# Performance work log

Hardware: AMD Instinct MI355X
Metric: run time of the kernel (lower is better)

The kernel has to match this reference:

```python
import jax, jax.numpy as jnp
import numpy as np

N_NODES = 50000
N_EDGES = 400000
D = 512
LN_EPS = 1e-5


def setup_inputs() -> dict:
    key = jax.random.key(0)
    k0, k1, k2, k3 = jax.random.split(key, 4)
    x = jax.random.normal(k0, (N_NODES, D), dtype=jnp.float32)
    src = jax.random.randint(k1, (N_EDGES,), 0, N_NODES, dtype=jnp.int64)
    dst = jax.random.randint(k2, (N_EDGES,), 0, N_NODES, dtype=jnp.int64)
    W = jax.random.normal(k3, (D, D), dtype=jnp.float32) * 0.05
    b = jnp.zeros((D,), dtype=jnp.float32)
    gamma = jnp.ones((D,), dtype=jnp.float32)
    beta = jnp.zeros((D,), dtype=jnp.float32)
    return {"x": x, "W": W, "b": b, "gamma": gamma, "beta": beta, "src": src, "dst": dst}


def reference(x, W, b, gamma, beta, src, dst):
    n = x.shape[0]
    ones = jnp.ones(src.shape, dtype=x.dtype)
    # DGL GraphConv norm='both': clamp degrees to >= 1
    deg_out = jnp.clip(jax.ops.segment_sum(ones, src, num_segments=n), 1.0)  # [N]
    deg_in = jnp.clip(jax.ops.segment_sum(ones, dst, num_segments=n), 1.0)   # [N]
    h = x * jax.lax.rsqrt(deg_out)[:, None]                 # [N, D] src normalization
    agg = jax.ops.segment_sum(h[src], dst, num_segments=n)  # gather->scatter-add SpMM
    h = agg * jax.lax.rsqrt(deg_in)[:, None]                # dst normalization
    h = h @ W + b                                           # dense linear
    # LayerNorm over last dim
    mu = jnp.mean(h, axis=-1, keepdims=True)
    var = jnp.mean(jnp.square(h - mu), axis=-1, keepdims=True)
    h = (h - mu) * jax.lax.rsqrt(var + LN_EPS) * gamma + beta
    # torch nn.GELU default = exact erf GELU
    return jax.nn.gelu(h, approximate=False)
```

## Files before the change

kernel.cpp:

```cpp
#include <hip/hip_runtime.h>
#include <hip/hip_bf16.h>

#define D 512

typedef __attribute__((ext_vector_type(8))) short bf16x8;
typedef __attribute__((ext_vector_type(4))) float f32x4;

__device__ inline float b2f(short h) {
    union { unsigned u; float f; } c;
    c.u = ((unsigned)(unsigned short)h) << 16;
    return c.f;
}

__global__ void k_hist(const int* __restrict__ src, const int* __restrict__ dst,
                       int* __restrict__ deg_out, int* __restrict__ deg_in, int E) {
    int e = blockIdx.x * 256 + threadIdx.x;
    if (e < E) {
        atomicAdd(&deg_out[src[e]], 1);
        atomicAdd(&deg_in[dst[e]], 1);
    }
}

__global__ __launch_bounds__(256)
void k_scale(const float* __restrict__ x, const int* __restrict__ deg_out,
             __hip_bfloat16* __restrict__ xs, int total16) {
    int i = blockIdx.x * 256 + threadIdx.x;
    if (i >= total16) return;
    int node = i >> 6;
    float w = rsqrtf((float)max(deg_out[node], 1));
    const float4* p = (const float4*)(x + (size_t)i * 8);
    float4 a = p[0], b = p[1];
    union { float4 f4; __hip_bfloat16 h[8]; } o;
    o.h[0] = __float2bfloat16(a.x * w);
    o.h[1] = __float2bfloat16(a.y * w);
    o.h[2] = __float2bfloat16(a.z * w);
    o.h[3] = __float2bfloat16(a.w * w);
    o.h[4] = __float2bfloat16(b.x * w);
    o.h[5] = __float2bfloat16(b.y * w);
    o.h[6] = __float2bfloat16(b.z * w);
    o.h[7] = __float2bfloat16(b.w * w);
    *(float4*)(xs + (size_t)i * 8) = o.f4;
}

__global__ void k_scan1(const int* __restrict__ deg_in, int* __restrict__ row_start,
                        int* __restrict__ partials, int N) {
    __shared__ int sm[1024];
    int tid = threadIdx.x;
    int i = blockIdx.x * 1024 + tid;
    int v = (i < N) ? deg_in[i] : 0;
    sm[tid] = v;
    __syncthreads();
    int acc = v;
    #pragma unroll
    for (int off = 1; off < 1024; off <<= 1) {
        int t = (tid >= off) ? sm[tid - off] : 0;
        __syncthreads();
        acc += t;
        sm[tid] = acc;
        __syncthreads();
    }
    if (i < N) row_start[i] = acc - v;
    if (tid == 1023) partials[blockIdx.x] = acc;
}

__global__ void k_scan2w(int* __restrict__ partials, int* __restrict__ row_start,
                         int nb, int N) {
    int lane = threadIdx.x;
    int orig = (lane < nb) ? partials[lane] : 0;
    int v = orig;
    #pragma unroll
    for (int off = 1; off < 64; off <<= 1) {
        int t = __shfl_up(v, off, 64);
        if (lane >= off) v += t;
    }
    if (lane < nb) partials[lane] = v - orig;
    if (lane == 63) row_start[N] = v;
}

__global__ void k_scan2s(int* __restrict__ partials, int* __restrict__ row_start,
                         int nb, int N) {
    if (threadIdx.x == 0 && blockIdx.x == 0) {
        int run = 0;
        for (int b = 0; b < nb; b++) { int t = partials[b]; partials[b] = run; run += t; }
        row_start[N] = run;
    }
}

__global__ void k_scan3(int* __restrict__ row_start, const int* __restrict__ partials, int N) {
    int i = blockIdx.x * 256 + threadIdx.x;
    if (i < N) row_start[i] += partials[i >> 10];
}

__global__ void k_fill(const int* __restrict__ src, const int* __restrict__ dst,
                       const int* __restrict__ row_start, int* __restrict__ cursor,
                       int* __restrict__ csr_src, int E) {
    int e = blockIdx.x * 256 + threadIdx.x;
    if (e < E) {
        int d = dst[e];
        int slot = atomicAdd(&cursor[d], 1);
        csr_src[row_start[d] + slot] = src[e];
    }
}

__global__ __launch_bounds__(256)
void k_spmm(const __hip_bfloat16* __restrict__ xs, const int* __restrict__ row_start,
            const int* __restrict__ csr_src, __hip_bfloat16* __restrict__ A, int N) {
    int wid = threadIdx.x >> 6;
    int lane = threadIdx.x & 63;
    int node = blockIdx.x * 4 + wid;
    if (node >= N) return;
    int rs = row_start[node], re = row_start[node + 1];

    float acc[8];
    #pragma unroll
    for (int k = 0; k < 8; k++) acc[k] = 0.f;
    const __hip_bfloat16* xl = xs + (size_t)lane * 8;

    int j = rs;
    for (; j + 4 <= re; j += 4) {
        int s0 = csr_src[j], s1 = csr_src[j + 1], s2 = csr_src[j + 2], s3 = csr_src[j + 3];
        bf16x8 v0 = *(const bf16x8*)(xl + (size_t)s0 * D);
        bf16x8 v1 = *(const bf16x8*)(xl + (size_t)s1 * D);
        bf16x8 v2 = *(const bf16x8*)(xl + (size_t)s2 * D);
        bf16x8 v3 = *(const bf16x8*)(xl + (size_t)s3 * D);
        #pragma unroll
        for (int k = 0; k < 8; k++)
            acc[k] += (b2f(v0[k]) + b2f(v1[k])) + (b2f(v2[k]) + b2f(v3[k]));
    }
    for (; j < re; j++) {
        int s = csr_src[j];
        bf16x8 v = *(const bf16x8*)(xl + (size_t)s * D);
        #pragma unroll
        for (int k = 0; k < 8; k++) acc[k] += b2f(v[k]);
    }

    float rn = rsqrtf((float)max(re - rs, 1));
    union { float4 f4; __hip_bfloat16 h[8]; } o;
    #pragma unroll
    for (int k = 0; k < 8; k++) o.h[k] = __float2bfloat16(acc[k] * rn);
    *(float4*)(A + (size_t)node * D + lane * 8) = o.f4;
}

__global__ __launch_bounds__(256)
void k_spmm_f32(const float* __restrict__ x, const int* __restrict__ row_start,
                const int* __restrict__ csr_src, const int* __restrict__ deg_out,
                __hip_bfloat16* __restrict__ A, int N) {
    int wid = threadIdx.x >> 6;
    int lane = threadIdx.x & 63;
    int node = blockIdx.x * 4 + wid;
    if (node >= N) return;
    int rs = row_start[node], re = row_start[node + 1];
    float4 acc0 = {0.f, 0.f, 0.f, 0.f};
    float4 acc1 = {0.f, 0.f, 0.f, 0.f};
    const float* xl = x + (size_t)lane * 8;
    for (int j = rs; j < re; j++) {
        int s = csr_src[j];
        float w = rsqrtf((float)max(deg_out[s], 1));
        const float4* p = (const float4*)(xl + (size_t)s * D);
        float4 a = p[0], b = p[1];
        acc0.x += a.x * w; acc0.y += a.y * w; acc0.z += a.z * w; acc0.w += a.w * w;
        acc1.x += b.x * w; acc1.y += b.y * w; acc1.z += b.z * w; acc1.w += b.w * w;
    }
    float rn = rsqrtf((float)max(re - rs, 1));
    union { float4 f4; __hip_bfloat16 h[8]; } o;
    o.h[0] = __float2bfloat16(acc0.x * rn);
    o.h[1] = __float2bfloat16(acc0.y * rn);
    o.h[2] = __float2bfloat16(acc0.z * rn);
    o.h[3] = __float2bfloat16(acc0.w * rn);
    o.h[4] = __float2bfloat16(acc1.x * rn);
    o.h[5] = __float2bfloat16(acc1.y * rn);
    o.h[6] = __float2bfloat16(acc1.z * rn);
    o.h[7] = __float2bfloat16(acc1.w * rn);
    *(float4*)(A + (size_t)node * D + lane * 8) = o.f4;
}

__global__ void k_packw(const float* __restrict__ W, __hip_bfloat16* __restrict__ Wp) {
    int tile = blockIdx.x;
    int lane = threadIdx.x;
    int kt = tile >> 5, nt = tile & 31;
    int k0 = kt * 32 + (lane >> 4) * 8;
    int n  = nt * 16 + (lane & 15);
    union { float4 f4; __hip_bfloat16 h[8]; } o;
    #pragma unroll
    for (int j = 0; j < 8; j++)
        o.h[j] = __float2bfloat16(W[(size_t)(k0 + j) * D + n]);
    *(float4*)(Wp + ((size_t)tile * 64 + lane) * 8) = o.f4;
}

__global__ __launch_bounds__(512)
void k_gemm(const __hip_bfloat16* __restrict__ A, const __hip_bfloat16* __restrict__ Wp,
            const float* __restrict__ bias, const float* __restrict__ gamma,
            const float* __restrict__ beta, float* __restrict__ out, int M) {
    int tid = threadIdx.x;
    int wid = tid >> 6, lane = tid & 63;
    int wm = wid >> 2, wn = wid & 3;
    int m0 = blockIdx.x * 32 + wm * 16;
    int l4 = lane >> 4;
    int coll = lane & 15;

    int arow = m0 + coll;
    bool rowok = (arow < M);

    f32x4 acc[8];
    #pragma unroll
    for (int t = 0; t < 8; t++) acc[t] = (f32x4){0.f, 0.f, 0.f, 0.f};

    const bf16x8* wpb = (const bf16x8*)Wp;
    for (int kt = 0; kt < 16; kt++) {
        bf16x8 afrag;
        if (rowok) {
            afrag = *(const bf16x8*)(A + (size_t)arow * D + kt * 32 + l4 * 8);
        } else {
            afrag = (bf16x8){0,0,0,0,0,0,0,0};
        }
        const bf16x8* wp = wpb + ((size_t)(kt * 32 + wn * 8) * 64 + lane);
        #pragma unroll
        for (int t = 0; t < 8; t++) {
            bf16x8 bfrag = wp[(size_t)t * 64];
            acc[t] = __builtin_amdgcn_mfma_f32_16x16x32_bf16(afrag, bfrag, acc[t], 0, 0, 0);
        }
    }

    __shared__ float s_sum[32][4];
    __shared__ float s_sq[32][4];

    #pragma unroll
    for (int r = 0; r < 4; r++) {
        float s = 0.f, q = 0.f;
        #pragma unroll
        for (int t = 0; t < 8; t++) {
            int col = wn * 128 + t * 16 + coll;
            float v = acc[t][r] + bias[col];
            acc[t][r] = v;
            s += v; q += v * v;
        }
        #pragma unroll
        for (int off = 1; off < 16; off <<= 1) {
            s += __shfl_xor(s, off, 64);
            q += __shfl_xor(q, off, 64);
        }
        if (coll == 0) {
            int rb = wm * 16 + l4 * 4 + r;
            s_sum[rb][wn] = s;
            s_sq[rb][wn] = q;
        }
    }
    __syncthreads();

    #pragma unroll
    for (int r = 0; r < 4; r++) {
        int rb = wm * 16 + l4 * 4 + r;
        int gr = blockIdx.x * 32 + rb;
        if (gr >= M) continue;
        float s = s_sum[rb][0] + s_sum[rb][1] + s_sum[rb][2] + s_sum[rb][3];
        float q = s_sq[rb][0] + s_sq[rb][1] + s_sq[rb][2] + s_sq[rb][3];
        float mean = s * (1.0f / 512.0f);
        float var = q * (1.0f / 512.0f) - mean * mean;
        float rstd = rsqrtf(fmaxf(var, 0.f) + 1e-5f);
        #pragma unroll
        for (int t = 0; t < 8; t++) {
            int col = wn * 128 + t * 16 + coll;
            float y = (acc[t][r] - mean) * rstd * gamma[col] + beta[col];
            float g = 0.5f * y * (1.0f + erff(y * 0.70710678118654752f));
            out[(size_t)gr * D + col] = g;
        }
    }
}

extern "C" void kernel_launch(void* const* d_in, const int* in_sizes, int n_in,
                              void* d_out, int out_size, void* d_ws, size_t ws_size,
                              hipStream_t stream) {
    const float* x     = (const float*)d_in[0];
    const float* W     = (const float*)d_in[1];
    const float* b     = (const float*)d_in[2];
    const float* gamma = (const float*)d_in[3];
    const float* beta  = (const float*)d_in[4];
    const int*   src   = (const int*)d_in[5];
    const int*   dst   = (const int*)d_in[6];
    int N = in_sizes[0] / D;
    int E = in_sizes[5];
    float* out = (float*)d_out;

    int* deg_out   = (int*)d_ws;
    int* deg_in    = deg_out + N;
    int* row_start = deg_in + N;
    int* cursor    = row_start + N + 1;
    int* partials  = cursor + N;
    int* csr_src   = partials + 64;
    uintptr_t p = (uintptr_t)(csr_src + E);
    p = (p + 255) & ~(uintptr_t)255;
    __hip_bfloat16* A = (__hip_bfloat16*)p;
    p += (size_t)N * D * sizeof(__hip_bfloat16);
    p = (p + 255) & ~(uintptr_t)255;
    __hip_bfloat16* Wp = (__hip_bfloat16*)p;
    p += (size_t)D * D * sizeof(__hip_bfloat16);
    p = (p + 255) & ~(uintptr_t)255;
    __hip_bfloat16* xs = (__hip_bfloat16*)p;
    size_t need_xs = (p - (uintptr_t)d_ws) + (size_t)N * D * sizeof(__hip_bfloat16);
    bool use_bf16_gather = (ws_size >= need_xs);

    hipMemsetAsync(deg_out, 0, (size_t)2 * N * sizeof(int), stream);
    hipMemsetAsync(cursor, 0, (size_t)N * sizeof(int), stream);

    k_hist<<<(E + 255) / 256, 256, 0, stream>>>(src, dst, deg_out, deg_in, E);
    int nb1 = (N + 1023) / 1024;
    k_scan1<<<nb1, 1024, 0, stream>>>(deg_in, row_start, partials, N);
    if (nb1 <= 64)
        k_scan2w<<<1, 64, 0, stream>>>(partials, row_start, nb1, N);
    else
        k_scan2s<<<1, 64, 0, stream>>>(partials, row_start, nb1, N);
    k_scan3<<<(N + 255) / 256, 256, 0, stream>>>(row_start, partials, N);
    k_fill<<<(E + 255) / 256, 256, 0, stream>>>(src, dst, row_start, cursor, csr_src, E);

    if (use_bf16_gather) {
        int total16 = N * 64;
        k_scale<<<(total16 + 255) / 256, 256, 0, stream>>>(x, deg_out, xs, total16);
        k_spmm<<<(N + 3) / 4, 256, 0, stream>>>(xs, row_start, csr_src, A, N);
    } else {
        k_spmm_f32<<<(N + 3) / 4, 256, 0, stream>>>(x, row_start, csr_src, deg_out, A, N);
    }
    k_packw<<<512, 64, 0, stream>>>(W, Wp);
    k_gemm<<<(N + 31) / 32, 512, 0, stream>>>(A, Wp, b, gamma, beta, out, N);
}
```

Before: 275.1 us.

## Stage W tiles in LDS with double buffering and widen GEMM tile to 64 rows

The fused GEMM+LayerNorm+GELU kernel now processes 64 rows per block, with each wave computing two 16-row fragments. Packed W k-slices are staged into a double-buffered 64KB LDS buffer via global_load_lds, so each B fragment read from LDS feeds two MFMAs. The exact erf GELU is replaced by a sigmoid-based polynomial approximation using exp2 and a fast reciprocal. The large LDS footprint and per-k-step barriers may limit occupancy, and the GELU approximation changes numerical accuracy.

```diff
diff --git a/kernel.cpp b/kernel.cpp
--- a/kernel.cpp
+++ b/kernel.cpp
@@ -10,6 +10,11 @@
     union { unsigned u; float f; } c;
     c.u = ((unsigned)(unsigned short)h) << 16;
     return c.f;
+}
+
+__device__ __forceinline__ void stage16(const void* g, void* l) {
+    __builtin_amdgcn_global_load_lds((const __attribute__((address_space(1))) void*)g,
+                                     (__attribute__((address_space(3))) void*)l, 16, 0, 0);
 }
 
 __global__ void k_hist(const int* __restrict__ src, const int* __restrict__ dst,
@@ -187,82 +192,117 @@
     *(float4*)(Wp + ((size_t)tile * 64 + lane) * 8) = o.f4;
 }
 
-__global__ __launch_bounds__(512)
+__global__ __launch_bounds__(512, 4)
 void k_gemm(const __hip_bfloat16* __restrict__ A, const __hip_bfloat16* __restrict__ Wp,
             const float* __restrict__ bias, const float* __restrict__ gamma,
             const float* __restrict__ beta, float* __restrict__ out, int M) {
+    __shared__ __align__(16) char smem[65536];
+    __shared__ float s_sum[64][4];
+    __shared__ float s_sq[64][4];
+
     int tid = threadIdx.x;
     int wid = tid >> 6, lane = tid & 63;
-    int wm = wid >> 2, wn = wid & 3;
-    int m0 = blockIdx.x * 32 + wm * 16;
-    int l4 = lane >> 4;
-    int coll = lane & 15;
-
-    int arow = m0 + coll;
-    bool rowok = (arow < M);
-
-    f32x4 acc[8];
-    #pragma unroll
-    for (int t = 0; t < 8; t++) acc[t] = (f32x4){0.f, 0.f, 0.f, 0.f};
-
-    const bf16x8* wpb = (const bf16x8*)Wp;
+    int wm = wid >> 1 & 0 ? 0 : (wid >> 2);
+    wm = wid >> 2;
+    int wn = wid & 3;
+    int l4 = lane >> 4, coll = lane & 15;
+    int bm0 = blockIdx.x * 64;
+
+    int arow0 = bm0 + wm * 16 + coll;
+    int arow1 = arow0 + 32;
+    if (arow0 > M - 1) arow0 = M - 1;
+    if (arow1 > M - 1) arow1 = M - 1;
+    const bf16x8* a0p = (const bf16x8*)(A + (size_t)arow0 * D + l4 * 8);
+    const bf16x8* a1p = (const bf16x8*)(A + (size_t)arow1 * D + l4 * 8);
+
+    int c0 = wid * 4;
+    const __hip_bfloat16* gbase = Wp + (size_t)c0 * 512 + lane * 8;
+    char* lds_c0 = smem + c0 * 1024;
+
+    f32x4 acc0[8], acc1[8];
+    #pragma unroll
+    for (int t = 0; t < 8; t++) { acc0[t] = (f32x4){0,0,0,0}; acc1[t] = (f32x4){0,0,0,0}; }
+
+    #pragma unroll
+    for (int r = 0; r < 4; r++)
+        stage16(gbase + r * 512, lds_c0 + r * 1024);
+    __syncthreads();
+
     for (int kt = 0; kt < 16; kt++) {
-        bf16x8 afrag;
-        if (rowok) {
-            afrag = *(const bf16x8*)(A + (size_t)arow * D + kt * 32 + l4 * 8);
-        } else {
-            afrag = (bf16x8){0,0,0,0,0,0,0,0};
+        int cur = (kt & 1) << 15;
+        bf16x8 a0 = a0p[kt * 4];
+        bf16x8 a1 = a1p[kt * 4];
+        if (kt < 15) {
+            const __hip_bfloat16* g = gbase + (size_t)(kt + 1) * 16384;
+            char* lb = lds_c0 + (((kt + 1) & 1) << 15);
+            #pragma unroll
+            for (int r = 0; r < 4; r++)
+                stage16(g + r * 512, lb + r * 1024);
         }
-        const bf16x8* wp = wpb + ((size_t)(kt * 32 + wn * 8) * 64 + lane);
         #pragma unroll
         for (int t = 0; t < 8; t++) {
-            bf16x8 bfrag = wp[(size_t)t * 64];
-            acc[t] = __builtin_amdgcn_mfma_f32_16x16x32_bf16(afrag, bfrag, acc[t], 0, 0, 0);
+            bf16x8 bf = *(const bf16x8*)(smem + cur + (((wn * 8 + t) * 64 + lane) << 4));
+            acc0[t] = __builtin_amdgcn_mfma_f32_16x16x32_bf16(a0, bf, acc0[t], 0, 0, 0);
+            acc1[t] = __builtin_amdgcn_mfma_f32_16x16x32_bf16(a1, bf, acc1[t], 0, 0, 0);
         }
-    }
-
-    __shared__ float s_sum[32][4];
-    __shared__ float s_sq[32][4];
-
-    #pragma unroll
-    for (int r = 0; r < 4; r++) {
-        float s = 0.f, q = 0.f;
-        #pragma unroll
-        for (int t = 0; t < 8; t++) {
-            int col = wn * 128 + t * 16 + coll;
-            float v = acc[t][r] + bias[col];
-            acc[t][r] = v;
-            s += v; q += v * v;
+        __syncthreads();
+    }
+
+    float bia[8], gam[8], bet[8];
+    #pragma unroll
+    for (int t = 0; t < 8; t++) {
+        int col = wn * 128 + t * 16 + coll;
+        bia[t] = bias[col]; gam[t] = gamma[col]; bet[t] = beta[col];
+    }
+    #pragma unroll
+    for (int f = 0; f < 2; f++) {
+        f32x4* acc = f ? acc1 : acc0;
+        #pragma unroll
+        for (int r = 0; r < 4; r++) {
+            float s = 0.f, q = 0.f;
+            #pragma unroll
+            for (int t = 0; t < 8; t++) {
+                float v = acc[t][r] + bia[t];
+                acc[t][r] = v;
+                s += v; q += v * v;
+            }
+            #pragma unroll
+            for (int off = 1; off < 16; off <<= 1) {
+                s += __shfl_xor(s, off, 64);
+                q += __shfl_xor(q, off, 64);
+            }
+            if (coll == 0) {
+                int rb = wm * 16 + f * 32 + l4 * 4 + r;
+                s_sum[rb][wn] = s;
+                s_sq[rb][wn] = q;
+            }
         }
-        #pragma unroll
-        for (int off = 1; off < 16; off <<= 1) {
-            s += __shfl_xor(s, off, 64);
-            q += __shfl_xor(q, off, 64);
-        }
-        if (coll == 0) {
-            int rb = wm * 16 + l4 * 4 + r;
-            s_sum[rb][wn] = s;
-            s_sq[rb][wn] = q;
-        }
     }
     __syncthreads();
 
     #pragma unroll
-    for (int r = 0; r < 4; r++) {
-        int rb = wm * 16 + l4 * 4 + r;
-        int gr = blockIdx.x * 32 + rb;
-        if (gr >= M) continue;
-        float s = s_sum[rb][0] + s_sum[rb][1] + s_sum[rb][2] + s_sum[rb][3];
-        float q = s_sq[rb][0] + s_sq[rb][1] + s_sq[rb][2] + s_sq[rb][3];
-        float mean = s * (1.0f / 512.0f);
-        float var = q * (1.0f / 512.0f) - mean * mean;
-        float rstd = rsqrtf(fmaxf(var, 0.f) + 1e-5f);
-        #pragma unroll
-        for (int t = 0; t < 8; t++) {
-            int col = wn * 128 + t * 16 + coll;
-            float y = (acc[t][r] - mean) * rstd * gamma[col] + beta[col];
-            float g = 0.5f * y * (1.0f + erff(y * 0.70710678118654752f));
-            out[(size_t)gr * D + col] = g;
+    for (int f = 0; f < 2; f++) {
+        f32x4* acc = f ? acc1 : acc0;
+        #pragma unroll
+        for (int r = 0; r < 4; r++) {
+            int rb = wm * 16 + f * 32 + l4 * 4 + r;
+            int gr = bm0 + rb;
+            if (gr >= M) continue;
+            float s = s_sum[rb][0] + s_sum[rb][1] + s_sum[rb][2] + s_sum[rb][3];
+            float q = s_sq[rb][0] + s_sq[rb][1] + s_sq[rb][2] + s_sq[rb][3];
+            float mean = s * (1.0f / 512.0f);
+            float var = q * (1.0f / 512.0f) - mean * mean;
+            float rstd = rsqrtf(fmaxf(var, 0.f) + 1e-5f);
+            float* orow = out + (size_t)gr * D + wn * 128 + coll;
+            #pragma unroll
+            for (int t = 0; t < 8; t++) {
+                float y = (acc[t][r] - mean) * rstd * gam[t] + bet[t];
+                float yy = y * y;
+                float pz = fmaf(yy, -0.1029423374f, -2.3022076728f);
+                float e = __builtin_amdgcn_exp2f(y * pz);
+                float g = y * __builtin_amdgcn_rcpf(1.0f + e);
+                orow[t * 16] = g;
+            }
         }
     }
 }
@@ -320,5 +360,5 @@
         k_spmm_f32<<<(N + 3) / 4, 256, 0, stream>>>(x, row_start, csr_src, deg_out, A, N);
     }
     k_packw<<<512, 64, 0, stream>>>(W, Wp);
-    k_gemm<<<(N + 31) / 32, 512, 0, stream>>>(A, Wp, b, gamma, beta, out, N);
-}
+    k_gemm<<<(N + 63) / 64, 512, 0, stream>>>(A, Wp, b, gamma, beta, out, N);
+}
```

Measured after the change: 247.1 us. -10.2%, faster.

## Split GEMM into LDS-staged persistent kernel plus separate LayerNorm-GELU pass

Applied to the files above, without the earlier changes.

Replaces the fused register-only GEMM with a persistent kernel. Each block keeps a 128-column slice of packed W resident in LDS and streams 192-row A tiles through double-buffered global_load_lds staging, with explicit waitcnt and barrier pipelining. The GEMM writes a bf16 intermediate that a separate row-wise LayerNorm+GELU kernel reads back. GELU now uses an exp2/rcp sigmoid-style approximation instead of erff. This aims to cut the redundant global reads of W per 32-row block, at the cost of an extra bf16 round trip through memory and some approximation error in GELU.

```diff
diff --git a/kernel.cpp b/kernel.cpp
--- a/kernel.cpp
+++ b/kernel.cpp
@@ -10,6 +10,11 @@
     union { unsigned u; float f; } c;
     c.u = ((unsigned)(unsigned short)h) << 16;
     return c.f;
+}
+
+__device__ __forceinline__ void stage16(const void* g, void* l) {
+    __builtin_amdgcn_global_load_lds((const __attribute__((address_space(1))) void*)g,
+                                     (__attribute__((address_space(3))) void*)l, 16, 0, 0);
 }
 
 __global__ void k_hist(const int* __restrict__ src, const int* __restrict__ dst,
@@ -174,6 +179,19 @@
     *(float4*)(A + (size_t)node * D + lane * 8) = o.f4;
 }
 
+__global__ void k_packw2(const float* __restrict__ W, __hip_bfloat16* __restrict__ Wp) {
+    int bid = blockIdx.x;
+    int c = bid >> 7, kt = (bid >> 3) & 15, ntc = bid & 7;
+    int lane = threadIdx.x;
+    int k0 = kt * 32 + (lane >> 4) * 8;
+    int n  = (c * 8 + ntc) * 16 + (lane & 15);
+    union { float4 f4; __hip_bfloat16 h[8]; } o;
+    #pragma unroll
+    for (int j = 0; j < 8; j++)
+        o.h[j] = __float2bfloat16(W[(size_t)(k0 + j) * D + n]);
+    *(float4*)(Wp + ((size_t)bid * 64 + lane) * 8) = o.f4;
+}
+
 __global__ void k_packw(const float* __restrict__ W, __hip_bfloat16* __restrict__ Wp) {
     int tile = blockIdx.x;
     int lane = threadIdx.x;
@@ -187,17 +205,206 @@
     *(float4*)(Wp + ((size_t)tile * 64 + lane) * 8) = o.f4;
 }
 
+__global__ __launch_bounds__(512, 2)
+void k_gemm2(const __hip_bfloat16* __restrict__ A, const __hip_bfloat16* __restrict__ Wp,
+             const float* __restrict__ bias, __hip_bfloat16* __restrict__ h, int M) {
+    __shared__ __align__(16) char lds[131072 + 2 * 12288];
+    char* ldsW = lds;
+    char* ldsA = lds + 131072;
+
+    int tid = threadIdx.x;
+    int wid = tid >> 6, lane = tid & 63;
+    int wr = wid >> 1, wc = wid & 1;
+    int l4 = lane >> 4, coll = lane & 15;
+    int cch = blockIdx.x & 3;
+    int rgrp = blockIdx.x >> 2;
+
+    {
+        const char* g = (const char*)Wp + (size_t)cch * 131072 + (size_t)wid * 1024 + lane * 16;
+        char* l = ldsW + wid * 1024;
+        #pragma unroll
+        for (int r = 0; r < 16; r++)
+            stage16(g + r * 8192, l + r * 8192);
+    }
+
+    int s0 = (wid < 4) ? wid : wid + 4;
+    int j0 = s0 / 3, rb0 = s0 % 3;
+    int s1 = wid + 4;
+    int j1 = s1 / 3, rb1 = s1 % 3;
+
+    float bia[4];
+    #pragma unroll
+    for (int ni = 0; ni < 4; ni++)
+        bia[ni] = bias[cch * 128 + wc * 64 + ni * 16 + coll];
+
+    int ntiles = (M + 191) / 192;
+
+    auto stageA = [&](int tb, int kt, int buf) {
+        char* bb = ldsA + buf * 12288;
+        {
+            int grow = tb + rb0 * 64 + lane;
+            if (grow > M - 1) grow = M - 1;
+            stage16((const char*)A + (size_t)grow * 1024 + kt * 64 + j0 * 16,
+                    bb + s0 * 1024);
+        }
+        if (wid < 4) {
+            int grow = tb + rb1 * 64 + lane;
+            if (grow > M - 1) grow = M - 1;
+            stage16((const char*)A + (size_t)grow * 1024 + kt * 64 + j1 * 16,
+                    bb + s1 * 1024);
+        }
+    };
+
+    for (int t = rgrp; t < ntiles; t += 64) {
+        int tb = t * 192;
+        stageA(tb, 0, 0);
+        stageA(tb, 1, 1);
+        if (wid < 4) { asm volatile("s_waitcnt vmcnt(2)" ::: "memory"); }
+        else         { asm volatile("s_waitcnt vmcnt(1)" ::: "memory"); }
+        __builtin_amdgcn_sched_barrier(0);
+        __builtin_amdgcn_s_barrier();
+
+        f32x4 acc[3][4];
+        #pragma unroll
+        for (int ai = 0; ai < 3; ai++)
+            #pragma unroll
+            for (int ni = 0; ni < 4; ni++) acc[ai][ni] = (f32x4){0.f, 0.f, 0.f, 0.f};
+
+        #pragma unroll
+        for (int kt = 0; kt < 14; kt++) {
+            int cur = kt & 1;
+            char* aw = ldsA + cur * 12288 + l4 * 3072 + (wr * 48 + coll) * 16;
+            bf16x8 af[3];
+            #pragma unroll
+            for (int ai = 0; ai < 3; ai++)
+                af[ai] = *(const bf16x8*)(aw + ai * 256);
+            char* ww = ldsW + (((kt * 8 + wc * 4) * 64) + lane) * 16;
+            bf16x8 bf[4];
+            #pragma unroll
+            for (int ni = 0; ni < 4; ni++)
+                bf[ni] = *(const bf16x8*)(ww + ni * 1024);
+            asm volatile("s_waitcnt lgkmcnt(0)" ::: "memory");
+            __builtin_amdgcn_sched_barrier(0);
+            __builtin_amdgcn_s_barrier();
+            stageA(tb, kt + 2, cur);
+            #pragma unroll
+            for (int ai = 0; ai < 3; ai++)
+                #pragma unroll
+                for (int ni = 0; ni < 4; ni++)
+                    acc[ai][ni] = __builtin_amdgcn_mfma_f32_16x16x32_bf16(af[ai], bf[ni], acc[ai][ni], 0, 0, 0);
+            if (wid < 4) { asm volatile("s_waitcnt vmcnt(2)" ::: "memory"); }
+            else         { asm volatile("s_waitcnt vmcnt(1)" ::: "memory"); }
+            __builtin_amdgcn_sched_barrier(0);
+            __builtin_amdgcn_s_barrier();
+        }
+        {
+            char* aw = ldsA + 0 * 12288 + l4 * 3072 + (wr * 48 + coll) * 16;
+            bf16x8 af[3];
+            #pragma unroll
+            for (int ai = 0; ai < 3; ai++) af[ai] = *(const bf16x8*)(aw + ai * 256);
+            char* ww = ldsW + (((14 * 8 + wc * 4) * 64) + lane) * 16;
+            #pragma unroll
+            for (int ni = 0; ni < 4; ni++) {
+                bf16x8 bf = *(const bf16x8*)(ww + ni * 1024);
+                #pragma unroll
+                for (int ai = 0; ai < 3; ai++)
+                    acc[ai][ni] = __builtin_amdgcn_mfma_f32_16x16x32_bf16(af[ai], bf, acc[ai][ni], 0, 0, 0);
+            }
+            asm volatile("s_waitcnt vmcnt(0)" ::: "memory");
+            __builtin_amdgcn_sched_barrier(0);
+            __builtin_amdgcn_s_barrier();
+        }
+        {
+            char* aw = ldsA + 1 * 12288 + l4 * 3072 + (wr * 48 + coll) * 16;
+            bf16x8 af[3];
+            #pragma unroll
+            for (int ai = 0; ai < 3; ai++) af[ai] = *(const bf16x8*)(aw + ai * 256);
+            char* ww = ldsW + (((15 * 8 + wc * 4) * 64) + lane) * 16;
+            bf16x8 bf[4];
+            #pragma unroll
+            for (int ni = 0; ni < 4; ni++) bf[ni] = *(const bf16x8*)(ww + ni * 1024);
+            asm volatile("s_waitcnt lgkmcnt(0)" ::: "memory");
+            __builtin_amdgcn_sched_barrier(0);
+            __builtin_amdgcn_s_barrier();
+            #pragma unroll
+            for (int ai = 0; ai < 3; ai++)
+                #pragma unroll
+                for (int ni = 0; ni < 4; ni++)
+                    acc[ai][ni] = __builtin_amdgcn_mfma_f32_16x16x32_bf16(af[ai], bf[ni], acc[ai][ni], 0, 0, 0);
+        }
+
+        #pragma unroll
+        for (int ai = 0; ai < 3; ai++) {
+            #pragma unroll
+            for (int r = 0; r < 4; r++) {
+                int row = tb + wr * 48 + ai * 16 + l4 * 4 + r;
+                if (row < M) {
+                    __hip_bfloat16* hp = h + (size_t)row * D + cch * 128 + wc * 64 + coll;
+                    #pragma unroll
+                    for (int ni = 0; ni < 4; ni++)
+                        hp[ni * 16] = __float2bfloat16(acc[ai][ni][r] + bia[ni]);
+                }
+            }
+        }
+    }
+}
+
+__global__ __launch_bounds__(256)
+void k_lngelu(const __hip_bfloat16* __restrict__ h, const float* __restrict__ gamma,
+              const float* __restrict__ beta, float* __restrict__ out, int M) {
+    int gw = (blockIdx.x * 256 + threadIdx.x) >> 6;
+    int lane = threadIdx.x & 63;
+    int nw = (gridDim.x * 256) >> 6;
+
+    float g8[8], b8[8];
+    #pragma unroll
+    for (int k = 0; k < 8; k++) {
+        g8[k] = gamma[lane * 8 + k];
+        b8[k] = beta[lane * 8 + k];
+    }
+
+    for (int row = gw; row < M; row += nw) {
+        bf16x8 v = *(const bf16x8*)(h + (size_t)row * D + lane * 8);
+        float f[8];
+        float s = 0.f, q = 0.f;
+        #pragma unroll
+        for (int k = 0; k < 8; k++) {
+            f[k] = b2f(v[k]);
+            s += f[k]; q += f[k] * f[k];
+        }
+        #pragma unroll
+        for (int off = 1; off < 64; off <<= 1) {
+            s += __shfl_xor(s, off, 64);
+            q += __shfl_xor(q, off, 64);
+        }
+        float mean = s * (1.0f / 512.0f);
+        float var = q * (1.0f / 512.0f) - mean * mean;
+        float rstd = rsqrtf(fmaxf(var, 0.f) + 1e-5f);
+        float o[8];
+        #pragma unroll
+        for (int k = 0; k < 8; k++) {
+            float y = (f[k] - mean) * rstd * g8[k] + b8[k];
+            float yy = y * y;
+            float pz = fmaf(yy, -0.1029423374f, -2.3022076728f);
+            float e = __builtin_amdgcn_exp2f(y * pz);
+            o[k] = y * __builtin_amdgcn_rcpf(1.0f + e);
+        }
+        float* orow = out + (size_t)row * D + lane * 8;
+        *(float4*)orow = (float4){o[0], o[1], o[2], o[3]};
+        *(float4*)(orow + 4) = (float4){o[4], o[5], o[6], o[7]};
+    }
+}
+
 __global__ __launch_bounds__(512)
 void k_gemm(const __hip_bfloat16* __restrict__ A, const __hip_bfloat16* __restrict__ Wp,
             const float* __restrict__ bias, const float* __restrict__ gamma,
             const float* __restrict__ beta, float* __restrict__ out, int M) {
     int tid = threadIdx.x;
     int wid = tid >> 6, lane = tid & 63;
-    int wm = wid >> 2, wn = wid & 3;
+    int wm = wid >> 2;
+    int wn = wid & 3;
+    int l4 = lane >> 4, coll = lane & 15;
     int m0 = blockIdx.x * 32 + wm * 16;
-    int l4 = lane >> 4;
-    int coll = lane & 15;
-
     int arow = m0 + coll;
     bool rowok = (arow < M);
 
@@ -208,11 +415,8 @@
     const bf16x8* wpb = (const bf16x8*)Wp;
     for (int kt = 0; kt < 16; kt++) {
         bf16x8 afrag;
-        if (rowok) {
-            afrag = *(const bf16x8*)(A + (size_t)arow * D + kt * 32 + l4 * 8);
-        } else {
-            afrag = (bf16x8){0,0,0,0,0,0,0,0};
-        }
+        if (rowok) afrag = *(const bf16x8*)(A + (size_t)arow * D + kt * 32 + l4 * 8);
+        else afrag = (bf16x8){0,0,0,0,0,0,0,0};
         const bf16x8* wp = wpb + ((size_t)(kt * 32 + wn * 8) * 64 + lane);
         #pragma unroll
         for (int t = 0; t < 8; t++) {
@@ -220,10 +424,8 @@
             acc[t] = __builtin_amdgcn_mfma_f32_16x16x32_bf16(afrag, bfrag, acc[t], 0, 0, 0);
         }
     }
-
     __shared__ float s_sum[32][4];
     __shared__ float s_sq[32][4];
-
     #pragma unroll
     for (int r = 0; r < 4; r++) {
         float s = 0.f, q = 0.f;
@@ -246,7 +448,6 @@
         }
     }
     __syncthreads();
-
     #pragma unroll
     for (int r = 0; r < 4; r++) {
         int rb = wm * 16 + l4 * 4 + r;
@@ -261,8 +462,10 @@
         for (int t = 0; t < 8; t++) {
             int col = wn * 128 + t * 16 + coll;
             float y = (acc[t][r] - mean) * rstd * gamma[col] + beta[col];
-            float g = 0.5f * y * (1.0f + erff(y * 0.70710678118654752f));
-            out[(size_t)gr * D + col] = g;
+            float yy = y * y;
+            float pz = fmaf(yy, -0.1029423374f, -2.3022076728f);
+            float e = __builtin_amdgcn_exp2f(y * pz);
+            out[(size_t)gr * D + col] = y * __builtin_amdgcn_rcpf(1.0f + e);
         }
     }
 }
@@ -297,7 +500,7 @@
     p = (p + 255) & ~(uintptr_t)255;
     __hip_bfloat16* xs = (__hip_bfloat16*)p;
     size_t need_xs = (p - (uintptr_t)d_ws) + (size_t)N * D * sizeof(__hip_bfloat16);
-    bool use_bf16_gather = (ws_size >= need_xs);
+    bool use_bf16_path = (ws_size >= need_xs);
 
     hipMemsetAsync(deg_out, 0, (size_t)2 * N * sizeof(int), stream);
     hipMemsetAsync(cursor, 0, (size_t)N * sizeof(int), stream);
@@ -312,13 +515,17 @@
     k_scan3<<<(N + 255) / 256, 256, 0, stream>>>(row_start, partials, N);
     k_fill<<<(E + 255) / 256, 256, 0, stream>>>(src, dst, row_start, cursor, csr_src, E);
 
-    if (use_bf16_gather) {
+    if (use_bf16_path) {
         int total16 = N * 64;
         k_scale<<<(total16 + 255) / 256, 256, 0, stream>>>(x, deg_out, xs, total16);
         k_spmm<<<(N + 3) / 4, 256, 0, stream>>>(xs, row_start, csr_src, A, N);
+        k_packw2<<<512, 64, 0, stream>>>(W, Wp);
+        __hip_bfloat16* h = xs;
+        k_gemm2<<<256, 512, 0, stream>>>(A, Wp, b, h, N);
+        k_lngelu<<<1024, 256, 0, stream>>>(h, gamma, beta, out, N);
     } else {
         k_spmm_f32<<<(N + 3) / 4, 256, 0, stream>>>(x, row_start, csr_src, deg_out, A, N);
-    }
-    k_packw<<<512, 64, 0, stream>>>(W, Wp);
-    k_gemm<<<(N + 31) / 32, 512, 0, stream>>>(A, Wp, b, gamma, beta, out, N);
-}
+        k_packw<<<512, 64, 0, stream>>>(W, Wp);
+        k_gemm<<<(N + 31) / 32, 512, 0, stream>>>(A, Wp, b, gamma, beta, out, N);
+    }
+}
```

After: 248.9 us. 9.5% less time.

## Write SpMM output in MFMA fragment layout and tile GEMM at 64 rows

Applied to the files above, without the earlier changes.

The SpMM kernel now runs 16 nodes per block and writes aggregated rows straight into a 16-row fragment-packed layout. The new GEMM kernel can then load A fragments with fully coalesced 16-byte loads, and each wave computes two 16-row tiles so every W fragment load is reused twice. W is repacked to match, and exact erf GELU is replaced with a sigmoid-style exp2/rcp approximation. The approximation changes numerics slightly, and the extra accumulators raise register pressure.

```diff
diff --git a/kernel.cpp b/kernel.cpp
--- a/kernel.cpp
+++ b/kernel.cpp
@@ -102,12 +102,12 @@
     }
 }
 
-__global__ __launch_bounds__(256)
+__global__ __launch_bounds__(1024)
 void k_spmm(const __hip_bfloat16* __restrict__ xs, const int* __restrict__ row_start,
-            const int* __restrict__ csr_src, __hip_bfloat16* __restrict__ A, int N) {
+            const int* __restrict__ csr_src, __hip_bfloat16* __restrict__ Ap, int N) {
     int wid = threadIdx.x >> 6;
     int lane = threadIdx.x & 63;
-    int node = blockIdx.x * 4 + wid;
+    int node = blockIdx.x * 16 + wid;
     if (node >= N) return;
     int rs = row_start[node], re = row_start[node + 1];
 
@@ -138,7 +138,7 @@
     union { float4 f4; __hip_bfloat16 h[8]; } o;
     #pragma unroll
     for (int k = 0; k < 8; k++) o.h[k] = __float2bfloat16(acc[k] * rn);
-    *(float4*)(A + (size_t)node * D + lane * 8) = o.f4;
+    *(float4*)((char*)Ap + ((size_t)(node >> 4) * 1024 + lane * 16 + (node & 15)) * 16) = o.f4;
 }
 
 __global__ __launch_bounds__(256)
@@ -174,6 +174,19 @@
     *(float4*)(A + (size_t)node * D + lane * 8) = o.f4;
 }
 
+__global__ void k_packw2(const float* __restrict__ W, __hip_bfloat16* __restrict__ Wp) {
+    int bid = blockIdx.x;
+    int c = bid >> 7, kt = (bid >> 3) & 15, ntc = bid & 7;
+    int lane = threadIdx.x;
+    int k0 = kt * 32 + (lane >> 4) * 8;
+    int n  = (c * 8 + ntc) * 16 + (lane & 15);
+    union { float4 f4; __hip_bfloat16 h[8]; } o;
+    #pragma unroll
+    for (int j = 0; j < 8; j++)
+        o.h[j] = __float2bfloat16(W[(size_t)(k0 + j) * D + n]);
+    *(float4*)(Wp + ((size_t)bid * 64 + lane) * 8) = o.f4;
+}
+
 __global__ void k_packw(const float* __restrict__ W, __hip_bfloat16* __restrict__ Wp) {
     int tile = blockIdx.x;
     int lane = threadIdx.x;
@@ -187,17 +200,112 @@
     *(float4*)(Wp + ((size_t)tile * 64 + lane) * 8) = o.f4;
 }
 
+__global__ __launch_bounds__(512, 4)
+void k_gemm3(const __hip_bfloat16* __restrict__ Ap, const __hip_bfloat16* __restrict__ Wp,
+             const float* __restrict__ bias, const float* __restrict__ gamma,
+             const float* __restrict__ beta, float* __restrict__ out, int M) {
+    __shared__ float s_sum[64][4];
+    __shared__ float s_sq[64][4];
+
+    int tid = threadIdx.x;
+    int wid = tid >> 6, lane = tid & 63;
+    int wm = wid >> 2, wn = wid & 3;
+    int l4 = lane >> 4, coll = lane & 15;
+    int tb = blockIdx.x * 64;
+    int rgmax = ((M + 15) >> 4) - 1;
+
+    int rg0 = (tb >> 4) + wm * 2;
+    int rgA = min(rg0, rgmax);
+    int rgB = min(rg0 + 1, rgmax);
+    const char* a0 = (const char*)Ap + (size_t)rgA * 16384 + (size_t)lane * 16;
+    const char* a1 = (const char*)Ap + (size_t)rgB * 16384 + (size_t)lane * 16;
+    const char* wb = (const char*)Wp + ((size_t)(wn * 128) * 64 + lane) * 16;
+
+    f32x4 acc0[8], acc1[8];
+    #pragma unroll
+    for (int t = 0; t < 8; t++) { acc0[t] = (f32x4){0,0,0,0}; acc1[t] = (f32x4){0,0,0,0}; }
+
+    for (int kt = 0; kt < 16; kt++) {
+        bf16x8 af0 = *(const bf16x8*)(a0 + (size_t)kt * 1024);
+        bf16x8 af1 = *(const bf16x8*)(a1 + (size_t)kt * 1024);
+        const char* wk = wb + (size_t)kt * 8192;
+        #pragma unroll
+        for (int t = 0; t < 8; t++) {
+            bf16x8 bf = *(const bf16x8*)(wk + (size_t)t * 1024);
+            acc0[t] = __builtin_amdgcn_mfma_f32_16x16x32_bf16(af0, bf, acc0[t], 0, 0, 0);
+            acc1[t] = __builtin_amdgcn_mfma_f32_16x16x32_bf16(af1, bf, acc1[t], 0, 0, 0);
+        }
+    }
+
+    float bia[8], gam[8], bet[8];
+    #pragma unroll
+    for (int t = 0; t < 8; t++) {
+        int col = wn * 128 + t * 16 + coll;
+        bia[t] = bias[col]; gam[t] = gamma[col]; bet[t] = beta[col];
+    }
+    #pragma unroll
+    for (int ai = 0; ai < 2; ai++) {
+        f32x4* acc = ai ? acc1 : acc0;
+        #pragma unroll
+        for (int r = 0; r < 4; r++) {
+            float s = 0.f, q = 0.f;
+            #pragma unroll
+            for (int t = 0; t < 8; t++) {
+                float v = acc[t][r] + bia[t];
+                acc[t][r] = v;
+                s += v; q += v * v;
+            }
+            #pragma unroll
+            for (int off = 1; off < 16; off <<= 1) {
+                s += __shfl_xor(s, off, 64);
+                q += __shfl_xor(q, off, 64);
+            }
+            if (coll == 0) {
+                int rb = wm * 32 + ai * 16 + l4 * 4 + r;
+                s_sum[rb][wn] = s;
+                s_sq[rb][wn] = q;
+            }
+        }
+    }
+    __syncthreads();
+
+    #pragma unroll
+    for (int ai = 0; ai < 2; ai++) {
+        f32x4* acc = ai ? acc1 : acc0;
+        #pragma unroll
+        for (int r = 0; r < 4; r++) {
+            int rb = wm * 32 + ai * 16 + l4 * 4 + r;
+            int gr = tb + rb;
+            if (gr >= M) continue;
+            float s = s_sum[rb][0] + s_sum[rb][1] + s_sum[rb][2] + s_sum[rb][3];
+            float q = s_sq[rb][0] + s_sq[rb][1] + s_sq[rb][2] + s_sq[rb][3];
+            float mean = s * (1.0f / 512.0f);
+            float var = q * (1.0f / 512.0f) - mean * mean;
+            float rstd = rsqrtf(fmaxf(var, 0.f) + 1e-5f);
+            float* orow = out + (size_t)gr * D + wn * 128 + coll;
+            #pragma unroll
+            for (int t = 0; t < 8; t++) {
+                float y = (acc[t][r] - mean) * rstd * gam[t] + bet[t];
+                float yy = y * y;
+                float pz = fmaf(yy, -0.1029423374f, -2.3022076728f);
+                float e = __builtin_amdgcn_exp2f(y * pz);
+                float g = y * __builtin_amdgcn_rcpf(1.0f + e);
+                orow[t * 16] = g;
+            }
+        }
+    }
+}
+
 __global__ __launch_bounds__(512)
 void k_gemm(const __hip_bfloat16* __restrict__ A, const __hip_bfloat16* __restrict__ Wp,
             const float* __restrict__ bias, const float* __restrict__ gamma,
             const float* __restrict__ beta, float* __restrict__ out, int M) {
     int tid = threadIdx.x;
     int wid = tid >> 6, lane = tid & 63;
-    int wm = wid >> 2, wn = wid & 3;
+    int wm = wid >> 2;
+    int wn = wid & 3;
+    int l4 = lane >> 4, coll = lane & 15;
     int m0 = blockIdx.x * 32 + wm * 16;
-    int l4 = lane >> 4;
-    int coll = lane & 15;
-
     int arow = m0 + coll;
     bool rowok = (arow < M);
 
@@ -208,11 +316,8 @@
     const bf16x8* wpb = (const bf16x8*)Wp;
     for (int kt = 0; kt < 16; kt++) {
         bf16x8 afrag;
-        if (rowok) {
-            afrag = *(const bf16x8*)(A + (size_t)arow * D + kt * 32 + l4 * 8);
-        } else {
-            afrag = (bf16x8){0,0,0,0,0,0,0,0};
-        }
+        if (rowok) afrag = *(const bf16x8*)(A + (size_t)arow * D + kt * 32 + l4 * 8);
+        else afrag = (bf16x8){0,0,0,0,0,0,0,0};
         const bf16x8* wp = wpb + ((size_t)(kt * 32 + wn * 8) * 64 + lane);
         #pragma unroll
         for (int t = 0; t < 8; t++) {
@@ -220,10 +325,8 @@
             acc[t] = __builtin_amdgcn_mfma_f32_16x16x32_bf16(afrag, bfrag, acc[t], 0, 0, 0);
         }
     }
-
     __shared__ float s_sum[32][4];
     __shared__ float s_sq[32][4];
-
     #pragma unroll
     for (int r = 0; r < 4; r++) {
         float s = 0.f, q = 0.f;
@@ -246,7 +349,6 @@
         }
     }
     __syncthreads();
-
     #pragma unroll
     for (int r = 0; r < 4; r++) {
         int rb = wm * 16 + l4 * 4 + r;
@@ -261,8 +363,10 @@
         for (int t = 0; t < 8; t++) {
             int col = wn * 128 + t * 16 + coll;
             float y = (acc[t][r] - mean) * rstd * gamma[col] + beta[col];
-            float g = 0.5f * y * (1.0f + erff(y * 0.70710678118654752f));
-            out[(size_t)gr * D + col] = g;
+            float yy = y * y;
+            float pz = fmaf(yy, -0.1029423374f, -2.3022076728f);
+            float e = __builtin_amdgcn_exp2f(y * pz);
+            out[(size_t)gr * D + col] = y * __builtin_amdgcn_rcpf(1.0f + e);
         }
     }
 }
@@ -290,14 +394,14 @@
     uintptr_t p = (uintptr_t)(csr_src + E);
     p = (p + 255) & ~(uintptr_t)255;
     __hip_bfloat16* A = (__hip_bfloat16*)p;
-    p += (size_t)N * D * sizeof(__hip_bfloat16);
+    p += (size_t)(((N + 15) / 16) * 16) * D * sizeof(__hip_bfloat16);
     p = (p + 255) & ~(uintptr_t)255;
     __hip_bfloat16* Wp = (__hip_bfloat16*)p;
     p += (size_t)D * D * sizeof(__hip_bfloat16);
     p = (p + 255) & ~(uintptr_t)255;
     __hip_bfloat16* xs = (__hip_bfloat16*)p;
     size_t need_xs = (p - (uintptr_t)d_ws) + (size_t)N * D * sizeof(__hip_bfloat16);
-    bool use_bf16_gather = (ws_size >= need_xs);
+    bool use_bf16_path = (ws_size >= need_xs);
 
     hipMemsetAsync(deg_out, 0, (size_t)2 * N * sizeof(int), stream);
     hipMemsetAsync(cursor, 0, (size_t)N * sizeof(int), stream);
@@ -312,13 +416,15 @@
     k_scan3<<<(N + 255) / 256, 256, 0, stream>>>(row_start, partials, N);
     k_fill<<<(E + 255) / 256, 256, 0, stream>>>(src, dst, row_start, cursor, csr_src, E);
 
-    if (use_bf16_gather) {
+    if (use_bf16_path) {
         int total16 = N * 64;
         k_scale<<<(total16 + 255) / 256, 256, 0, stream>>>(x, deg_out, xs, total16);
-        k_spmm<<<(N + 3) / 4, 256, 0, stream>>>(xs, row_start, csr_src, A, N);
+        k_spmm<<<(N + 15) / 16, 1024, 0, stream>>>(xs, row_start, csr_src, A, N);
+        k_packw2<<<512, 64, 0, stream>>>(W, Wp);
+        k_gemm3<<<(N + 63) / 64, 512, 0, stream>>>(A, Wp, b, gamma, beta, out, N);
     } else {
         k_spmm_f32<<<(N + 3) / 4, 256, 0, stream>>>(x, row_start, csr_src, deg_out, A, N);
-    }
-    k_packw<<<512, 64, 0, stream>>>(W, Wp);
-    k_gemm<<<(N + 31) / 32, 512, 0, stream>>>(A, Wp, b, gamma, beta, out, N);
-}
+        k_packw<<<512, 64, 0, stream>>>(W, Wp);
+        k_gemm<<<(N + 31) / 32, 512, 0, stream>>>(A, Wp, b, gamma, beta, out, N);
+    }
+}
```

Result: faster. 240.6 us (-12.6%).
